# Kernel tuning notes

Hardware: AMD Instinct MI355X
Metric: run time of the kernel (lower is better)

The kernel has to match this reference:

```python
import jax, jax.numpy as jnp
import numpy as np

H = 56; W = 56; WS = 7; SHIFT = 3; C = 128; NH = 4; HD = C // NH
N = WS * WS; NW = (H // WS) * (W // WS); B = 64; HID = 4 * C
ALPHA = (1, 2, 4, 8); SCALE = HD ** -0.5


def _rel_index_np():
    coords = np.stack(np.meshgrid(np.arange(WS), np.arange(WS), indexing="ij"))
    cf = coords.reshape(2, -1)
    rel = (cf[:, :, None] - cf[:, None, :]).transpose(1, 2, 0).copy()
    rel[:, :, 0] += WS - 1
    rel[:, :, 1] += WS - 1
    rel[:, :, 0] *= 2 * WS - 1
    return rel.sum(-1).astype(np.int32)  # (N, N)


def _attn_mask_np():
    img = np.zeros((1, H, W, 1), np.float32)
    cnt = 0
    sl = (slice(0, -WS), slice(-WS, -SHIFT), slice(-SHIFT, None))
    for hs in sl:
        for ws in sl:
            img[:, hs, ws, :] = cnt
            cnt += 1
    mw = img.reshape(1, H // WS, WS, W // WS, WS, 1).transpose(0, 1, 3, 2, 4, 5).reshape(-1, N)
    am = mw[:, None, :] - mw[:, :, None]
    return np.where(am != 0, -100.0, 0.0).astype(np.float32)  # (NW, N, N)


def setup_inputs() -> dict:
    key = jax.random.key(0)
    ks = jax.random.split(key, 8)
    p = lambda k, shp, s=0.02: jax.random.normal(k, shp, jnp.float32) * s
    return {
        "x": jax.random.normal(ks[0], (B, H * W, C), jnp.float32),
        "gumbel_weights": jax.nn.softmax(jax.random.normal(ks[1], (4,), jnp.float32)),
        "norm1_w": jnp.ones((C,), jnp.float32), "norm1_b": jnp.zeros((C,), jnp.float32),
        "qkv_w": p(ks[2], (3 * C, C)), "qkv_b": jnp.zeros((3 * C,), jnp.float32),
        "rel_bias_table": p(ks[3], ((2 * WS - 1) ** 2, NH)),
        "proj_w": p(ks[4], (C, C)), "proj_b": jnp.zeros((C,), jnp.float32),
        "attn_mask": jnp.asarray(_attn_mask_np()),
        "norm2_w": jnp.ones((C,), jnp.float32), "norm2_b": jnp.zeros((C,), jnp.float32),
        "fc1_w": p(ks[5], (HID, C)), "fc1_b": jnp.zeros((HID,), jnp.float32),
        "fc2_w": p(ks[6], (C, HID)), "fc2_b": jnp.zeros((C,), jnp.float32),
        "rel_index": jnp.asarray(_rel_index_np()),
    }


def _ln(x, w, b, eps=1e-5):
    mu = x.mean(-1, keepdims=True)
    var = ((x - mu) ** 2).mean(-1, keepdims=True)
    return (x - mu) * jax.lax.rsqrt(var + eps) * w + b


def _win_part(x):  # (B,H,W,C) -> (B*NW, N, C)
    b = x.shape[0]
    x = x.reshape(b, H // WS, WS, W // WS, WS, C).transpose(0, 1, 3, 2, 4, 5)
    return x.reshape(-1, N, C)


def _win_rev(w, b):  # (b*NW, N, C) -> (b,H,W,C)
    x = w.reshape(b, H // WS, W // WS, WS, WS, C).transpose(0, 1, 3, 2, 4, 5)
    return x.reshape(b, H, W, C)


def _window_attn(xw, qkv_w, qkv_b, bias, mask, proj_w, proj_b):
    b = xw.shape[0]
    qkv = (xw @ qkv_w.T + qkv_b).reshape(b, N, 3, NH, HD).transpose(2, 0, 3, 1, 4)
    q, k, v = qkv[0] * SCALE, qkv[1], qkv[2]  # (b,NH,N,HD)
    a = jnp.einsum("bhnd,bhmd->bhnm", q, k) + bias[None]
    a = (a.reshape(b // NW, NW, NH, N, N) + mask[None, :, None]).reshape(b, NH, N, N)
    a = jax.nn.softmax(a, axis=-1)
    o = jnp.einsum("bhnm,bhmd->bhnd", a, v).transpose(0, 2, 1, 3).reshape(b, N, C)
    return o @ proj_w.T + proj_b


def _forward(x, gw, n1w, n1b, qkv_w, qkv_b, rbt, pw, pb, am, n2w, n2b, f1w, f1b, f2w, f2b, rel_index):
    shortcut = x
    xs = _ln(x, n1w, n1b).reshape(B, H, W, C)
    xs = jnp.roll(xs, (-SHIFT, -SHIFT), axis=(1, 2))  # cyclic shift
    xw = _win_part(xs)  # (B*NW, N, C)
    bias = rbt[rel_index.reshape(-1)].reshape(N, N, NH).transpose(2, 0, 1)  # (NH,N,N)
    half = xw.shape[0] // 2
    xw_l, xw_s = xw[:half], xw[half:]
    # large half: full-width window attention
    y_l = _window_attn(xw_l, qkv_w, qkv_b, bias, am, pw, pb)
    # small half: gumbel-gated slimmable branches (zero channels beyond C//alpha in/out)
    ch = jnp.arange(C)
    y_s = jnp.zeros_like(xw_s)
    for i, a in enumerate(ALPHA):
        if a > NH:
            continue
        cm = (ch < C // a).astype(xw.dtype)
        yb = _window_attn(xw_s * cm, qkv_w, qkv_b, bias, am, pw, pb) * cm
        y_s = y_s + yb * gw[i]
    attn_out = jnp.concatenate([y_l, y_s], axis=0)
    xr = _win_rev(attn_out, B)
    xr = jnp.roll(xr, (SHIFT, SHIFT), axis=(1, 2)).reshape(B, H * W, C)
    x = shortcut + xr
    # MLP with gumbel-gated slimmable small half (matches Mlp.forward)
    xn = _ln(x, n2w, n2b)
    xn_l, xn_s = xn[: B // 2], xn[B // 2 :]
    m_l = jax.nn.gelu(xn_l @ f1w.T + f1b, approximate=False) @ f2w.T + f2b
    m_s = jnp.zeros_like(xn_s)
    for i, a in enumerate(ALPHA):
        if a > NH:
            continue
        cm = (ch < C // a).astype(xn.dtype)
        yb = (jax.nn.gelu((xn_s * cm) @ f1w.T + f1b, approximate=False) @ f2w.T + f2b) * cm
        m_s = m_s + yb * gw[i]
    mlp_out = jnp.concatenate([m_l, m_s], axis=0)
    return x + mlp_out


def reference(x, gumbel_weights, norm1_w, norm1_b, qkv_w, qkv_b, rel_bias_table, proj_w, proj_b, attn_mask, norm2_w, norm2_b, fc1_w, fc1_b, fc2_w, fc2_b, rel_index):
    return _forward(x, gumbel_weights, norm1_w, norm1_b, qkv_w, qkv_b, rel_bias_table, proj_w, proj_b, attn_mask, norm2_w, norm2_b, fc1_w, fc1_b, fc2_w, fc2_b, rel_index)
```

## Files before the change

### kernel.cpp

```cpp
#include <hip/hip_runtime.h>
#include <hip/hip_bf16.h>

#define SHIFT_ 3
#define SCALE_ 0.17677669529663687f
#define NTOK   200704
#define NWIN   4096

typedef short v8s __attribute__((ext_vector_type(8)));
typedef float v4f __attribute__((ext_vector_type(4)));
#define MFMA16(a, b, c) __builtin_amdgcn_mfma_f32_16x16x32_bf16(a, b, c, 0, 0, 0)

static __device__ __forceinline__ unsigned short f2bf(float f) {
    union { float f; unsigned int u; } v; v.f = f;
    unsigned int u = v.u;
    unsigned int r = u + 0x7FFFu + ((u >> 16) & 1u);
    return (unsigned short)(r >> 16);
}
static __device__ __forceinline__ float wsum(float v) {
    #pragma unroll
    for (int o = 32; o; o >>= 1) v += __shfl_xor(v, o);
    return v;
}

#define WS_COMB  67108864
#define WS_WQKV  71303168
#define WS_WPROJ 71401472
#define WS_F1W   71434240
#define WS_F2W   71565312

__global__ __launch_bounds__(256) void k_prep(
    const float* __restrict__ amask, const float* __restrict__ rbt,
    const int* __restrict__ relidx,
    const float* __restrict__ qkvw, const float* __restrict__ projw,
    const float* __restrict__ f1w, const float* __restrict__ f2w,
    float* __restrict__ comb, unsigned short* __restrict__ wqkv,
    unsigned short* __restrict__ wproj, unsigned short* __restrict__ f1wb,
    unsigned short* __restrict__ f2wb, unsigned short* __restrict__ xw) {
    int idx = blockIdx.x * 256 + threadIdx.x;
    if (idx < 1048576) {
        int wpos = idx >> 14;
        int h = (idx >> 12) & 3;
        int i = (idx >> 6) & 63;
        int j = idx & 63;
        float v;
        if (j >= 49) v = -1e30f;
        else if (i >= 49) v = 0.f;
        else v = amask[wpos * 2401 + i * 49 + j] + rbt[relidx[i * 49 + j] * 4 + h];
        comb[idx] = v;
    } else if (idx < 1048576 + 49152) {
        int k = idx - 1048576; wqkv[k] = f2bf(qkvw[k]);
    } else if (idx < 1048576 + 49152 + 16384) {
        int k = idx - (1048576 + 49152); wproj[k] = f2bf(projw[k]);
    } else if (idx < 1048576 + 49152 + 16384 + 65536) {
        int k = idx - (1048576 + 49152 + 16384); f1wb[k] = f2bf(f1w[k]);
    } else if (idx < 1048576 + 49152 + 16384 + 65536 + 65536) {
        int k = idx - (1048576 + 49152 + 16384 + 65536); f2wb[k] = f2bf(f2w[k]);
    } else {
        int k = idx - 1245184;
        if (k < 983040) {
            int win = k / 240, r = k - win * 240;
            uint4 z = make_uint4(0u, 0u, 0u, 0u);
            *(uint4*)((char*)xw + (size_t)win * 16384 + 12544 + (size_t)r * 16) = z;
        }
    }
}

__global__ __launch_bounds__(256) void k_ln1(const float* __restrict__ x,
                                             const float* __restrict__ nw,
                                             const float* __restrict__ nb,
                                             unsigned short* __restrict__ xw) {
    int tok  = blockIdx.x * 4 + (threadIdx.x >> 6);
    int lane = threadIdx.x & 63;
    int win = tok / 49, t = tok - win * 49;
    int bb = win >> 6, wh = (win >> 3) & 7, ww = win & 7;
    int i = t / 7, j = t - i * 7;
    int h  = wh * 7 + i + SHIFT_; if (h  >= 56) h  -= 56;
    int w2 = ww * 7 + j + SHIFT_; if (w2 >= 56) w2 -= 56;
    const float* src = x + ((size_t)bb * 3136 + h * 56 + w2) * 128;
    float v0 = src[lane], v1 = src[lane + 64];
    float mu = wsum(v0 + v1) * (1.f / 128.f);
    float d0 = v0 - mu, d1 = v1 - mu;
    float var = wsum(d0 * d0 + d1 * d1) * (1.f / 128.f);
    float inv = rsqrtf(var + 1e-5f);
    unsigned short* dst = xw + (size_t)win * 8192 + t * 128;
    dst[lane]      = f2bf(d0 * inv * nw[lane]      + nb[lane]);
    dst[lane + 64] = f2bf(d1 * inv * nw[lane + 64] + nb[lane + 64]);
}

__global__ __launch_bounds__(256) void k_ln2(const float* __restrict__ x2,
                                             const float* __restrict__ nw,
                                             const float* __restrict__ nb,
                                             unsigned short* __restrict__ xn) {
    int tok  = blockIdx.x * 4 + (threadIdx.x >> 6);
    int lane = threadIdx.x & 63;
    const float* src = x2 + (size_t)tok * 128;
    float v0 = src[lane], v1 = src[lane + 64];
    float mu = wsum(v0 + v1) * (1.f / 128.f);
    float d0 = v0 - mu, d1 = v1 - mu;
    float var = wsum(d0 * d0 + d1 * d1) * (1.f / 128.f);
    float inv = rsqrtf(var + 1e-5f);
    unsigned short* dst = xn + (size_t)tok * 128;
    dst[lane]      = f2bf(d0 * inv * nw[lane]      + nb[lane]);
    dst[lane + 64] = f2bf(d1 * inv * nw[lane + 64] + nb[lane + 64]);
}

template<int KA>
__device__ __forceinline__ void attn_pass(
    const v8s (&ax)[4][4],
    const unsigned short* __restrict__ wqkv, const float* __restrict__ qkvb,
    const float* __restrict__ comb,
    const unsigned short* __restrict__ wproj, const float* __restrict__ pbias,
    float wgt, int wpos, int wv, int li, int lg,
    unsigned short* __restrict__ s_q, unsigned short* __restrict__ s_k,
    unsigned short* __restrict__ s_v, unsigned short* __restrict__ pw_,
    v4f (&yacc)[2][4])
{
    const v4f z4 = {0.f, 0.f, 0.f, 0.f};
    constexpr int Ca = KA * 32;

    #pragma unroll 2
    for (int nt = 0; nt < 6; nt++) {
        const int ntg = wv * 6 + nt, o0 = ntg * 16;
        v4f acc[4] = {z4, z4, z4, z4};
        #pragma unroll
        for (int k = 0; k < KA; k++) {
            v8s b = *(const v8s*)(wqkv + (o0 + li) * 128 + k * 32 + lg * 8);
            #pragma unroll
            for (int m = 0; m < 4; m++) acc[m] = MFMA16(ax[m][k], b, acc[m]);
        }
        float bo = qkvb[o0 + li];
        if (ntg < 16) {
            unsigned short* dst = (ntg < 8) ? s_q : s_k;
            const int oc = (ntg < 8) ? o0 : o0 - 128;
            const float scl = (ntg < 8) ? SCALE_ : 1.f;
            #pragma unroll
            for (int m = 0; m < 4; m++)
                #pragma unroll
                for (int r = 0; r < 4; r++)
                    dst[(m * 16 + lg * 4 + r) * 136 + oc + li] =
                        f2bf((acc[m][r] + bo) * scl);
        } else {
            const int d = (ntg - 16) * 16 + li;
            #pragma unroll
            for (int m = 0; m < 4; m++) {
                int t0_ = m * 16 + lg * 4;
                unsigned int p0 = (unsigned int)f2bf(acc[m][0] + bo) |
                                  ((unsigned int)f2bf(acc[m][1] + bo) << 16);
                unsigned int p1 = (unsigned int)f2bf(acc[m][2] + bo) |
                                  ((unsigned int)f2bf(acc[m][3] + bo) << 16);
                *(unsigned int*)(s_v + d * 72 + t0_)     = p0;
                *(unsigned int*)(s_v + d * 72 + t0_ + 2) = p1;
            }
        }
    }
    __syncthreads();

    v4f oacc[8];
    #pragma unroll
    for (int i = 0; i < 8; i++) oacc[i] = z4;
    #pragma unroll 2
    for (int h = 0; h < 4; h++) {
        v8s aq = *(const v8s*)(s_q + (wv * 16 + li) * 136 + h * 32 + lg * 8);
        v4f sc[4];
        #pragma unroll
        for (int ntj = 0; ntj < 4; ntj++) {
            v8s bk = *(const v8s*)(s_k + (ntj * 16 + li) * 136 + h * 32 + lg * 8);
            sc[ntj] = MFMA16(aq, bk, z4);
        }
        const float* cb = comb + ((size_t)(wpos * 4 + h) << 12) + (wv * 16 + lg * 4) * 64;
        #pragma unroll
        for (int r = 0; r < 4; r++) {
            float vmax = -3.0e38f, e[4];
            #pragma unroll
            for (int ntj = 0; ntj < 4; ntj++) {
                float v_ = sc[ntj][r] + cb[r * 64 + ntj * 16 + li];
                sc[ntj][r] = v_;
                vmax = fmaxf(vmax, v_);
            }
            #pragma unroll
            for (int o_ = 1; o_ < 16; o_ <<= 1) vmax = fmaxf(vmax, __shfl_xor(vmax, o_));
            float ssum = 0.f;
            #pragma unroll
            for (int ntj = 0; ntj < 4; ntj++) {
                e[ntj] = __expf(sc[ntj][r] - vmax);
                ssum += e[ntj];
            }
            #pragma unroll
            for (int o_ = 1; o_ < 16; o_ <<= 1) ssum += __shfl_xor(ssum, o_);
            float inv = __builtin_amdgcn_rcpf(ssum);
            #pragma unroll
            for (int ntj = 0; ntj < 4; ntj++)
                pw_[(lg * 4 + r) * 72 + ntj * 16 + li] = f2bf(e[ntj] * inv);
        }
        #pragma unroll
        for (int k0 = 0; k0 < 2; k0++) {
            v8s ap = *(const v8s*)(pw_ + li * 72 + k0 * 32 + lg * 8);
            #pragma unroll
            for (int dn = 0; dn < 2; dn++) {
                v8s bv = *(const v8s*)(s_v + (h * 32 + dn * 16 + li) * 72 + k0 * 32 + lg * 8);
                oacc[h * 2 + dn] = MFMA16(ap, bv, oacc[h * 2 + dn]);
            }
        }
    }
    __syncthreads();

    unsigned short* s_o = s_k;
    #pragma unroll
    for (int ot = 0; ot < 8; ot++)
        #pragma unroll
        for (int r = 0; r < 4; r++)
            s_o[(wv * 16 + lg * 4 + r) * 136 + ot * 16 + li] = f2bf(oacc[ot][r]);
    __syncthreads();

    if (KA == 4 || wv * 16 < Ca) {
        v8s ao[4][4];
        #pragma unroll
        for (int m = 0; m < 4; m++)
            #pragma unroll
            for (int k = 0; k < 4; k++)
                ao[m][k] = *(const v8s*)(s_o + (m * 16 + li) * 136 + k * 32 + lg * 8);
        #pragma unroll
        for (int nt = 0; nt < 2; nt++) {
            const int co0 = (nt * 4 + wv) * 16;
            if (nt == 0 || Ca == 128) {
                if (co0 < Ca) {
                    v4f pacc[4] = {z4, z4, z4, z4};
                    #pragma unroll
                    for (int k = 0; k < 4; k++) {
                        v8s b = *(const v8s*)(wproj + (co0 + li) * 128 + k * 32 + lg * 8);
                        #pragma unroll
                        for (int m = 0; m < 4; m++) pacc[m] = MFMA16(ao[m][k], b, pacc[m]);
                    }
                    float bo = pbias[co0 + li];
                    #pragma unroll
                    for (int m = 0; m < 4; m++)
                        #pragma unroll
                        for (int r = 0; r < 4; r++)
                            yacc[nt][m][r] += wgt * (pacc[m][r] + bo);
                }
            }
        }
    }
    __syncthreads();
}

__global__ __launch_bounds__(256, 2) void k_attn(
    const unsigned short* __restrict__ xw,
    const unsigned short* __restrict__ wqkv, const float* __restrict__ qkvb,
    const float* __restrict__ comb,
    const unsigned short* __restrict__ wproj, const float* __restrict__ pbias,
    const float* __restrict__ gw,
    const float* __restrict__ x, float* __restrict__ out) {

    __shared__ unsigned short sm[31232];
    unsigned short* s_q = sm;
    unsigned short* s_k = sm + 8704;
    unsigned short* s_v = sm + 17408;
    unsigned short* s_p = sm + 26624;

    const int tid = threadIdx.x, wv = tid >> 6, lane = tid & 63;
    const int li = lane & 15, lg = lane >> 4;
    const int w = blockIdx.x;
    const int wpos = w & 63;
    const bool sp = (w >= 2048);
    const unsigned short* xwin = xw + (size_t)w * 8192;
    unsigned short* pw_ = s_p + wv * 1152;

    const v4f z4 = {0.f, 0.f, 0.f, 0.f};
    v4f yacc[2][4];
    #pragma unroll
    for (int n = 0; n < 2; n++)
        #pragma unroll
        for (int m = 0; m < 4; m++) yacc[n][m] = z4;

    v8s ax[4][4];
    #pragma unroll
    for (int m = 0; m < 4; m++)
        #pragma unroll
        for (int k = 0; k < 4; k++)
            ax[m][k] = *(const v8s*)(xwin + (m * 16 + li) * 128 + k * 32 + lg * 8);

    if (sp) {
        attn_pass<4>(ax, wqkv, qkvb, comb, wproj, pbias, gw[0], wpos, wv, li, lg,
                     s_q, s_k, s_v, pw_, yacc);
        attn_pass<2>(ax, wqkv, qkvb, comb, wproj, pbias, gw[1], wpos, wv, li, lg,
                     s_q, s_k, s_v, pw_, yacc);
        attn_pass<1>(ax, wqkv, qkvb, comb, wproj, pbias, gw[2], wpos, wv, li, lg,
                     s_q, s_k, s_v, pw_, yacc);
    } else {
        attn_pass<4>(ax, wqkv, qkvb, comb, wproj, pbias, 1.f, wpos, wv, li, lg,
                     s_q, s_k, s_v, pw_, yacc);
    }

    const int bb = w >> 6, wh = (w >> 3) & 7, ww = w & 7;
    #pragma unroll
    for (int m = 0; m < 4; m++)
        #pragma unroll
        for (int r = 0; r < 4; r++) {
            int t = m * 16 + lg * 4 + r;
            if (t < 49) {
                int ti = t / 7, tj = t - ti * 7;
                int h2 = wh * 7 + ti + SHIFT_; if (h2 >= 56) h2 -= 56;
                int w2 = ww * 7 + tj + SHIFT_; if (w2 >= 56) w2 -= 56;
                size_t base = ((size_t)bb * 3136 + h2 * 56 + w2) * 128;
                #pragma unroll
                for (int nt = 0; nt < 2; nt++) {
                    int c = (nt * 4 + wv) * 16 + li;
                    out[base + c] = x[base + c] + yacc[nt][m][r];
                }
            }
        }
}

template<int KA>
__device__ __forceinline__ void mlp_pass(
    const v8s (&ax)[2][4],
    const unsigned short* __restrict__ f1wb, const float* __restrict__ f1b,
    const unsigned short* __restrict__ f2wb, const float* __restrict__ f2b,
    float wgt, int wv, int li, int lg,
    unsigned short* __restrict__ s_h, v4f (&yacc)[2][2])
{
    const v4f z4 = {0.f, 0.f, 0.f, 0.f};
    constexpr int Ca = KA * 32;

    #pragma unroll 4
    for (int nt = 0; nt < 8; nt++) {
        const int o0 = wv * 128 + nt * 16;
        v4f acc[2] = {z4, z4};
        #pragma unroll
        for (int k = 0; k < KA; k++) {
            v8s b = *(const v8s*)(f1wb + (o0 + li) * 128 + k * 32 + lg * 8);
            acc[0] = MFMA16(ax[0][k], b, acc[0]);
            acc[1] = MFMA16(ax[1][k], b, acc[1]);
        }
        float bo = f1b[o0 + li];
        #pragma unroll
        for (int m = 0; m < 2; m++)
            #pragma unroll
            for (int r = 0; r < 4; r++) {
                float v_ = acc[m][r] + bo;
                v_ = 0.5f * v_ * (1.f + erff(v_ * 0.70710678118654752f));
                s_h[(m * 16 + lg * 4 + r) * 520 + o0 + li] = f2bf(v_);
            }
    }
    __syncthreads();

    if (KA == 4) {
        const int c0 = wv * 16, c1 = 64 + wv * 16;
        v4f acc2[2][2] = {{z4, z4}, {z4, z4}};
        #pragma unroll
        for (int k = 0; k < 16; k++) {
            v8s a0 = *(const v8s*)(s_h + li * 520 + k * 32 + lg * 8);
            v8s a1 = *(const v8s*)(s_h + (16 + li) * 520 + k * 32 + lg * 8);
            v8s b0 = *(const v8s*)(f2wb + (c0 + li) * 512 + k * 32 + lg * 8);
            v8s b1 = *(const v8s*)(f2wb + (c1 + li) * 512 + k * 32 + lg * 8);
            acc2[0][0] = MFMA16(a0, b0, acc2[0][0]);
            acc2[0][1] = MFMA16(a1, b0, acc2[0][1]);
            acc2[1][0] = MFMA16(a0, b1, acc2[1][0]);
            acc2[1][1] = MFMA16(a1, b1, acc2[1][1]);
        }
        float bo0 = f2b[c0 + li], bo1 = f2b[c1 + li];
        #pragma unroll
        for (int m = 0; m < 2; m++)
            #pragma unroll
            for (int r = 0; r < 4; r++) {
                yacc[0][m][r] += wgt * (acc2[0][m][r] + bo0);
                yacc[1][m][r] += wgt * (acc2[1][m][r] + bo1);
            }
    } else if (KA == 2 || wv < 2) {
        const int c0 = wv * 16;
        v4f acc2[2] = {z4, z4};
        #pragma unroll
        for (int k = 0; k < 16; k++) {
            v8s a0 = *(const v8s*)(s_h + li * 520 + k * 32 + lg * 8);
            v8s a1 = *(const v8s*)(s_h + (16 + li) * 520 + k * 32 + lg * 8);
            v8s b0 = *(const v8s*)(f2wb + (c0 + li) * 512 + k * 32 + lg * 8);
            acc2[0] = MFMA16(a0, b0, acc2[0]);
            acc2[1] = MFMA16(a1, b0, acc2[1]);
        }
        float bo0 = f2b[c0 + li];
        #pragma unroll
        for (int m = 0; m < 2; m++)
            #pragma unroll
            for (int r = 0; r < 4; r++)
                yacc[0][m][r] += wgt * (acc2[m][r] + bo0);
    }
}

__global__ __launch_bounds__(256, 3) void k_mlp(
    const unsigned short* __restrict__ xn,
    const unsigned short* __restrict__ f1wb, const float* __restrict__ f1b,
    const unsigned short* __restrict__ f2wb, const float* __restrict__ f2b,
    const float* __restrict__ gw, float* __restrict__ out) {

    __shared__ unsigned short s_h[32 * 520];

    const int tid = threadIdx.x, wv = tid >> 6, lane = tid & 63;
    const int li = lane & 15, lg = lane >> 4;
    const int t0 = blockIdx.x * 32;
    const bool sp = (t0 >= 100352);

    const v4f z4 = {0.f, 0.f, 0.f, 0.f};
    v4f yacc[2][2];
    #pragma unroll
    for (int n = 0; n < 2; n++)
        #pragma unroll
        for (int m = 0; m < 2; m++) yacc[n][m] = z4;

    v8s ax[2][4];
    #pragma unroll
    for (int m = 0; m < 2; m++)
        #pragma unroll
        for (int k = 0; k < 4; k++)
            ax[m][k] = *(const v8s*)(xn + (size_t)(t0 + m * 16 + li) * 128 + k * 32 + lg * 8);

    if (sp) {
        mlp_pass<4>(ax, f1wb, f1b, f2wb, f2b, gw[0], wv, li, lg, s_h, yacc);
        __syncthreads();
        mlp_pass<2>(ax, f1wb, f1b, f2wb, f2b, gw[1], wv, li, lg, s_h, yacc);
        __syncthreads();
        mlp_pass<1>(ax, f1wb, f1b, f2wb, f2b, gw[2], wv, li, lg, s_h, yacc);
    } else {
        mlp_pass<4>(ax, f1wb, f1b, f2wb, f2b, 1.f, wv, li, lg, s_h, yacc);
    }

    #pragma unroll
    for (int nt = 0; nt < 2; nt++) {
        int co = (nt * 4 + wv) * 16 + li;
        #pragma unroll
        for (int m = 0; m < 2; m++)
            #pragma unroll
            for (int r = 0; r < 4; r++) {
                size_t oi = (size_t)(t0 + m * 16 + lg * 4 + r) * 128 + co;
                out[oi] += yacc[nt][m][r];
            }
    }
}

extern "C" void kernel_launch(void* const* d_in, const int* in_sizes, int n_in,
                              void* d_out, int out_size, void* d_ws, size_t ws_size,
                              hipStream_t stream) {
    const float* x      = (const float*)d_in[0];
    const float* gw     = (const float*)d_in[1];
    const float* n1w    = (const float*)d_in[2];
    const float* n1b    = (const float*)d_in[3];
    const float* qkvw   = (const float*)d_in[4];
    const float* qkvb   = (const float*)d_in[5];
    const float* rbt    = (const float*)d_in[6];
    const float* pw     = (const float*)d_in[7];
    const float* pb     = (const float*)d_in[8];
    const float* amask  = (const float*)d_in[9];
    const float* n2w    = (const float*)d_in[10];
    const float* n2b    = (const float*)d_in[11];
    const float* f1w    = (const float*)d_in[12];
    const float* f1b    = (const float*)d_in[13];
    const float* f2w    = (const float*)d_in[14];
    const float* f2b    = (const float*)d_in[15];
    const int*   relidx = (const int*)d_in[16];
    float* out = (float*)d_out;

    unsigned short* xw    = (unsigned short*)d_ws;
    float*          comb  = (float*)((char*)d_ws + WS_COMB);
    unsigned short* wqkv  = (unsigned short*)((char*)d_ws + WS_WQKV);
    unsigned short* wproj = (unsigned short*)((char*)d_ws + WS_WPROJ);
    unsigned short* f1wb  = (unsigned short*)((char*)d_ws + WS_F1W);
    unsigned short* f2wb  = (unsigned short*)((char*)d_ws + WS_F2W);
    unsigned short* xn    = (unsigned short*)d_ws;

    hipLaunchKernelGGL(k_prep, dim3(8704), dim3(256), 0, stream,
                       amask, rbt, relidx, qkvw, pw, f1w, f2w,
                       comb, wqkv, wproj, f1wb, f2wb, xw);
    hipLaunchKernelGGL(k_ln1, dim3(NTOK / 4), dim3(256), 0, stream, x, n1w, n1b, xw);
    hipLaunchKernelGGL(k_attn, dim3(NWIN), dim3(256), 0, stream,
                       xw, wqkv, qkvb, comb, wproj, pb, gw, x, out);
    hipLaunchKernelGGL(k_ln2, dim3(NTOK / 4), dim3(256), 0, stream, out, n2w, n2b, xn);
    hipLaunchKernelGGL(k_mlp, dim3(NTOK / 32), dim3(256), 0, stream,
                       xn, f1wb, f1b, f2wb, f2b, gw, out);
}
```

Baseline: 855.6 us.

## Reuse Q smem for softmax probabilities, raise occupancy, add MFMA priority hints

```diff
diff --git a/kernel.cpp b/kernel.cpp
--- a/kernel.cpp
+++ b/kernel.cpp
@@ -112,7 +112,7 @@
     const unsigned short* __restrict__ wproj, const float* __restrict__ pbias,
     float wgt, int wpos, int wv, int li, int lg,
     unsigned short* __restrict__ s_q, unsigned short* __restrict__ s_k,
-    unsigned short* __restrict__ s_v, unsigned short* __restrict__ pw_,
+    unsigned short* __restrict__ s_v,
     v4f (&yacc)[2][4])
 {
     const v4f z4 = {0.f, 0.f, 0.f, 0.f};
@@ -122,12 +122,14 @@
     for (int nt = 0; nt < 6; nt++) {
         const int ntg = wv * 6 + nt, o0 = ntg * 16;
         v4f acc[4] = {z4, z4, z4, z4};
+        __builtin_amdgcn_s_setprio(1);
         #pragma unroll
         for (int k = 0; k < KA; k++) {
             v8s b = *(const v8s*)(wqkv + (o0 + li) * 128 + k * 32 + lg * 8);
             #pragma unroll
             for (int m = 0; m < 4; m++) acc[m] = MFMA16(ax[m][k], b, acc[m]);
         }
+        __builtin_amdgcn_s_setprio(0);
         float bo = qkvb[o0 + li];
         if (ntg < 16) {
             unsigned short* dst = (ntg < 8) ? s_q : s_k;
@@ -155,25 +157,40 @@
     }
     __syncthreads();
 
+    v8s aq[4];
+    #pragma unroll
+    for (int h = 0; h < 4; h++)
+        aq[h] = *(const v8s*)(s_q + (wv * 16 + li) * 136 + h * 32 + lg * 8);
+    __syncthreads();
+
+    unsigned short* pw_ = s_q + wv * 1152;
+
     v4f oacc[8];
     #pragma unroll
     for (int i = 0; i < 8; i++) oacc[i] = z4;
     #pragma unroll 2
     for (int h = 0; h < 4; h++) {
-        v8s aq = *(const v8s*)(s_q + (wv * 16 + li) * 136 + h * 32 + lg * 8);
+        const float* cb = comb + ((size_t)(wpos * 4 + h) << 12) + (wv * 16 + lg * 4) * 64;
+        float cbr[4][4];
+        #pragma unroll
+        for (int r = 0; r < 4; r++)
+            #pragma unroll
+            for (int ntj = 0; ntj < 4; ntj++)
+                cbr[r][ntj] = cb[r * 64 + ntj * 16 + li];
         v4f sc[4];
+        __builtin_amdgcn_s_setprio(1);
         #pragma unroll
         for (int ntj = 0; ntj < 4; ntj++) {
             v8s bk = *(const v8s*)(s_k + (ntj * 16 + li) * 136 + h * 32 + lg * 8);
-            sc[ntj] = MFMA16(aq, bk, z4);
-        }
-        const float* cb = comb + ((size_t)(wpos * 4 + h) << 12) + (wv * 16 + lg * 4) * 64;
+            sc[ntj] = MFMA16(aq[h], bk, z4);
+        }
+        __builtin_amdgcn_s_setprio(0);
         #pragma unroll
         for (int r = 0; r < 4; r++) {
             float vmax = -3.0e38f, e[4];
             #pragma unroll
             for (int ntj = 0; ntj < 4; ntj++) {
-                float v_ = sc[ntj][r] + cb[r * 64 + ntj * 16 + li];
+                float v_ = sc[ntj][r] + cbr[r][ntj];
                 sc[ntj][r] = v_;
                 vmax = fmaxf(vmax, v_);
             }
@@ -192,6 +209,7 @@
             for (int ntj = 0; ntj < 4; ntj++)
                 pw_[(lg * 4 + r) * 72 + ntj * 16 + li] = f2bf(e[ntj] * inv);
         }
+        __builtin_amdgcn_s_setprio(1);
         #pragma unroll
         for (int k0 = 0; k0 < 2; k0++) {
             v8s ap = *(const v8s*)(pw_ + li * 72 + k0 * 32 + lg * 8);
@@ -201,6 +219,7 @@
                 oacc[h * 2 + dn] = MFMA16(ap, bv, oacc[h * 2 + dn]);
             }
         }
+        __builtin_amdgcn_s_setprio(0);
     }
     __syncthreads();
 
@@ -225,12 +244,14 @@
             if (nt == 0 || Ca == 128) {
                 if (co0 < Ca) {
                     v4f pacc[4] = {z4, z4, z4, z4};
+                    __builtin_amdgcn_s_setprio(1);
                     #pragma unroll
                     for (int k = 0; k < 4; k++) {
                         v8s b = *(const v8s*)(wproj + (co0 + li) * 128 + k * 32 + lg * 8);
                         #pragma unroll
                         for (int m = 0; m < 4; m++) pacc[m] = MFMA16(ao[m][k], b, pacc[m]);
                     }
+                    __builtin_amdgcn_s_setprio(0);
                     float bo = pbias[co0 + li];
                     #pragma unroll
                     for (int m = 0; m < 4; m++)
@@ -244,7 +265,7 @@
     __syncthreads();
 }
 
-__global__ __launch_bounds__(256, 2) void k_attn(
+__global__ __launch_bounds__(256, 3) void k_attn(
     const unsigned short* __restrict__ xw,
     const unsigned short* __restrict__ wqkv, const float* __restrict__ qkvb,
     const float* __restrict__ comb,
@@ -252,11 +273,10 @@
     const float* __restrict__ gw,
     const float* __restrict__ x, float* __restrict__ out) {
 
-    __shared__ unsigned short sm[31232];
+    __shared__ unsigned short sm[26624];
     unsigned short* s_q = sm;
     unsigned short* s_k = sm + 8704;
     unsigned short* s_v = sm + 17408;
-    unsigned short* s_p = sm + 26624;
 
     const int tid = threadIdx.x, wv = tid >> 6, lane = tid & 63;
     const int li = lane & 15, lg = lane >> 4;
@@ -264,7 +284,6 @@
     const int wpos = w & 63;
     const bool sp = (w >= 2048);
     const unsigned short* xwin = xw + (size_t)w * 8192;
-    unsigned short* pw_ = s_p + wv * 1152;
 
     const v4f z4 = {0.f, 0.f, 0.f, 0.f};
     v4f yacc[2][4];
@@ -282,14 +301,14 @@
 
     if (sp) {
         attn_pass<4>(ax, wqkv, qkvb, comb, wproj, pbias, gw[0], wpos, wv, li, lg,
-                     s_q, s_k, s_v, pw_, yacc);
+                     s_q, s_k, s_v, yacc);
         attn_pass<2>(ax, wqkv, qkvb, comb, wproj, pbias, gw[1], wpos, wv, li, lg,
-                     s_q, s_k, s_v, pw_, yacc);
+                     s_q, s_k, s_v, yacc);
         attn_pass<1>(ax, wqkv, qkvb, comb, wproj, pbias, gw[2], wpos, wv, li, lg,
-                     s_q, s_k, s_v, pw_, yacc);
+                     s_q, s_k, s_v, yacc);
     } else {
         attn_pass<4>(ax, wqkv, qkvb, comb, wproj, pbias, 1.f, wpos, wv, li, lg,
-                     s_q, s_k, s_v, pw_, yacc);
+                     s_q, s_k, s_v, yacc);
     }
 
     const int bb = w >> 6, wh = (w >> 3) & 7, ww = w & 7;
```

New measurement: 908.8 us. 1.06x slower.
